# Performance work log

Hardware: AMD Instinct MI355X
Metric: run time of the kernel (lower is better)

The kernel has to match this reference:

```python
import jax, jax.numpy as jnp
import numpy as np
from jax import lax

SHIFT_SIZE = 5
PAD = SHIFT_SIZE // 2


def _shift(xn, axis):
    """xn: (B, C, Hp, Wp, Dp) zero-padded volume. Split channels into
    SHIFT_SIZE chunks and roll each chunk by shift in [-PAD, PAD] along `axis`."""
    chunks = jnp.split(xn, SHIFT_SIZE, axis=1)
    shifted = [jnp.roll(c, s, axis=axis) for c, s in zip(chunks, range(-PAD, PAD + 1))]
    return jnp.concatenate(shifted, axis=1)


def _shift_tokens(x, H, W, D, axis):
    """x: (B, N, C) tokens -> shifted tokens (B, N, C). axis=2 shifts H, axis=3 shifts W."""
    B, N, C = x.shape
    xn = x.transpose(0, 2, 1).reshape(B, C, H, W, D)
    xn = jnp.pad(xn, ((0, 0), (0, 0), (PAD, PAD), (PAD, PAD), (PAD, PAD)))
    xs = _shift(xn, axis)
    xs = xs[:, :, PAD:PAD + H, PAD:PAD + W, PAD:PAD + D]
    return xs.reshape(B, C, N).transpose(0, 2, 1)


def setup_inputs() -> dict:
    key = jax.random.key(0)
    ks = jax.random.split(key, 4)
    B, H, W, D = 2, 32, 32, 32
    N = H * W * D
    Cin, Ch = 160, 640
    return {
        "x": jax.random.normal(ks[0], (B, N, Cin), jnp.float32),
        "fc1_w": jax.random.normal(ks[1], (Ch, Cin), jnp.float32) * 0.02,
        "fc1_b": jnp.zeros((Ch,), jnp.float32),
        "dw_w": jax.random.normal(ks[2], (Ch, 1, 3, 3, 3), jnp.float32) * (2.0 / 27.0) ** 0.5,
        "dw_b": jnp.zeros((Ch,), jnp.float32),
        "fc2_w": jax.random.normal(ks[3], (Cin, Ch), jnp.float32) * 0.02,
        "fc2_b": jnp.zeros((Cin,), jnp.float32),
        "H": H, "W": W, "D": D,
    }


def reference(x, fc1_w, fc1_b, dw_w, dw_b, fc2_w, fc2_b, H, W, D):
    B, N, Cin = x.shape
    Ch = fc1_w.shape[0]
    # shift block 1: roll along H (axis 2)
    xs = _shift_tokens(x, H, W, D, axis=2)
    # fc1
    h = jnp.einsum('bnc,hc->bnh', xs, fc1_w) + fc1_b  # (B, N, Ch)
    # depthwise 3x3x3 conv
    hv = h.transpose(0, 2, 1).reshape(B, Ch, H, W, D)
    hv = lax.conv_general_dilated(
        hv, dw_w, window_strides=(1, 1, 1), padding='SAME',
        feature_group_count=Ch,
        dimension_numbers=('NCDHW', 'OIDHW', 'NCDHW'))
    hv = hv + dw_b[None, :, None, None, None]
    hv = jax.nn.gelu(hv, approximate=False)
    h = hv.reshape(B, Ch, N).transpose(0, 2, 1)
    # shift block 2: roll along W (axis 3)
    hs = _shift_tokens(h, H, W, D, axis=3)
    # fc2
    out = jnp.einsum('bnh,oh->bno', hs, fc2_w) + fc2_b  # (B, N, Cin)
    return out
```

## Files before the change

### kernel.cpp

```cpp
#include <hip/hip_runtime.h>
#include <hip/hip_bf16.h>
#include <math.h>

#define DEVI __device__ __forceinline__

typedef _Float16 f16;
typedef f16 f16x2 __attribute__((ext_vector_type(2)));
typedef f16 f16x4 __attribute__((ext_vector_type(4)));
typedef f16 f16x8 __attribute__((ext_vector_type(8)));
typedef float f32x4 __attribute__((ext_vector_type(4)));

constexpr int Bb = 2, Hh = 32, Ww = 32, Dd = 32;
constexpr int Nn = Hh * Ww * Dd;
constexpr int BN = Bb * Nn;
constexpr int CIN = 160, CHH = 640;
constexpr int PD = 34;
constexpr int PT = PD * PD * PD;

constexpr size_t W1_OFF  = 0;
constexpr size_t W2_OFF  = W1_OFF + (size_t)CHH * CIN * 2;
constexpr size_t WTH_OFF = W2_OFF + (size_t)CIN * CHH * 2;
constexpr size_t ZP_OFF  = WTH_OFF + 34816;
constexpr size_t U_OFF   = 458752;
constexpr size_t H1P_OFF = U_OFF + (size_t)BN * CHH * 2;

DEVI void async16(const void* g, void* l) {
  __builtin_amdgcn_global_load_lds(
      (const __attribute__((address_space(1))) void*)g,
      (__attribute__((address_space(3))) void*)l, 16, 0, 0);
}

__global__ __launch_bounds__(256) void k_prep_w(const float* __restrict__ fc1w,
                                                const float* __restrict__ fc2w,
                                                const float* __restrict__ dww,
                                                f16* __restrict__ w1h,
                                                f16* __restrict__ w2h,
                                                f16* __restrict__ wTh,
                                                unsigned* __restrict__ zp) {
  int i = blockIdx.x * 256 + threadIdx.x;
  const int NW = CHH * CIN;
  if (i < NW) {
    w1h[i] = (f16)fc1w[i];
  } else if (i < 2 * NW) {
    int j = i - NW;
    w2h[j] = (f16)fc2w[j];
  } else if (i < 2 * NW + 27 * CHH) {
    int j = i - 2 * NW;
    int ch = j / 27, tap = j % 27;
    wTh[tap * CHH + ch] = (f16)dww[j];
  } else if (i < 2 * NW + 27 * CHH + 2048) {
    zp[i - (2 * NW + 27 * CHH)] = 0u;
  }
}

__global__ __launch_bounds__(256) void k_zero_pad(f16* __restrict__ h1p) {
  int g = blockIdx.x * 256 + threadIdx.x;
  int p = g / 80;
  int c = g - p * 80;
  if (p >= 2 * PT) return;
  int r = p % PT;
  int hp = r / (PD * PD);
  int r2 = r % (PD * PD);
  int wp = r2 / PD, dp = r2 % PD;
  bool pad = (hp == 0) | (hp == PD - 1) | (wp == 0) | (wp == PD - 1) |
             (dp == 0) | (dp == PD - 1);
  if (!pad) return;
  f16x8 z = {};
  *(f16x8*)&h1p[(size_t)p * CHH + c * 8] = z;
}

__global__ __launch_bounds__(256) void k_gemm1(const float* __restrict__ x,
                                               const f16* __restrict__ w1h,
                                               const float* __restrict__ fc1b,
                                               f16* __restrict__ h1p) {
  constexpr int LDA = 168;
  __shared__ f16 lsA[128 * LDA];
  __shared__ f16 lsB[128 * 32];
  const int tid = threadIdx.x;
  const int lane = tid & 63, wave = tid >> 6;
  const int row0 = blockIdx.x * 128;
  const int wr = wave >> 1, wc = wave & 1;
  const int rl = lane & 15, kb = (lane >> 4) * 8;

#pragma unroll
  for (int i = 0; i < 20; ++i) {
    int c = i * 256 + tid;
    int row = c / 40;
    int q = c - row * 40;
    int ch0 = q * 4;
    int ks = ch0 >> 5;
    int s = ks - 2;
    int t = row0 + row;
    int h = (t >> 10) & 31;
    int hs = h - s;
    float4 v = {0.f, 0.f, 0.f, 0.f};
    if (hs >= 0 && hs < 32)
      v = *(const float4*)&x[(long)(t - s * 1024) * CIN + ch0];
    f16x4 o4;
    o4[0] = (f16)v.x; o4[1] = (f16)v.y; o4[2] = (f16)v.z; o4[3] = (f16)v.w;
    *(f16x4*)&lsA[row * LDA + ch0] = o4;
  }
  __syncthreads();

  for (int nt = 0; nt < 5; ++nt) {
    const int col0 = nt * 128;
    f32x4 acc[4][4] = {};
    for (int ks = 0; ks < 5; ++ks) {
#pragma unroll
      for (int issue = 0; issue < 2; ++issue) {
        int c = issue * 256 + tid;
        int br = c >> 2;
        int kc = (c & 3) * 8;
        const f16* src = w1h + (size_t)(col0 + br) * CIN + ks * 32 + kc;
        async16(src, (char*)lsB + issue * 4096 + wave * 1024);
      }
      __syncthreads();
      f16x8 af[4], bfr[4];
#pragma unroll
      for (int mi = 0; mi < 4; ++mi)
        af[mi] = *(const f16x8*)&lsA[(wr * 64 + mi * 16 + rl) * LDA + ks * 32 + kb];
#pragma unroll
      for (int ni = 0; ni < 4; ++ni)
        bfr[ni] = *(const f16x8*)&lsB[(wc * 64 + ni * 16 + rl) * 32 + kb];
#pragma unroll
      for (int mi = 0; mi < 4; ++mi)
#pragma unroll
        for (int ni = 0; ni < 4; ++ni)
          acc[mi][ni] = __builtin_amdgcn_mfma_f32_16x16x32_f16(af[mi], bfr[ni], acc[mi][ni], 0, 0, 0);
      __syncthreads();
    }
    const int rq = lane >> 4;
#pragma unroll
    for (int mi = 0; mi < 4; ++mi) {
      int rowq = row0 + wr * 64 + mi * 16 + rq * 4;
      int bq = rowq >> 15;
      int nq = rowq & 32767;
      int hq = nq >> 10, wq = (nq >> 5) & 31, dq = nq & 31;
      size_t pos = (size_t)((bq * PD + hq + 1) * PD + (wq + 1)) * PD + (dq + 1);
      f16* dst0 = h1p + pos * CHH;
#pragma unroll
      for (int ni = 0; ni < 4; ++ni) {
        int col = col0 + wc * 64 + ni * 16 + rl;
        float bias = fc1b[col];
#pragma unroll
        for (int r = 0; r < 4; ++r)
          dst0[(size_t)r * CHH + col] = (f16)(acc[mi][ni][r] + bias);
      }
    }
  }
}

__global__ __launch_bounds__(256) void k_conv(const f16* __restrict__ h1p,
                                              const f16* __restrict__ wTh,
                                              const float* __restrict__ dwb,
                                              f16* __restrict__ h2h) {
  __shared__ f16 lw[27 * 64];
  __shared__ f16 lb[64];
  const int tid = threadIdx.x;
  const int cg = blockIdx.y;
#pragma unroll
  for (int i = 0; i < 7; ++i) {
    int idx = i * 256 + tid;
    if (idx < 27 * 64) lw[idx] = wTh[(idx >> 6) * CHH + cg * 64 + (idx & 63)];
  }
  if (tid < 64) lb[tid] = (f16)dwb[cg * 64 + tid];
  __syncthreads();

  const int lane = tid & 63, wave = tid >> 6;
  const int line = blockIdx.x * 4 + wave;
  const int c8 = lane & 7, dq = lane >> 3;
  const int d0 = dq * 4;
  const int ch0 = cg * 64 + c8 * 8;
  const int w = line & 31, h = (line >> 5) & 31, b = line >> 10;

  const size_t cidx = (size_t)((b * PD + h) * PD + w) * PD + d0;
  const f16* base = h1p + cidx * CHH + ch0;

  f16x8 acc[4];
  {
    f16x8 binit = *(const f16x8*)&lb[c8 * 8];
    acc[0] = binit; acc[1] = binit; acc[2] = binit; acc[3] = binit;
  }

#pragma unroll
  for (int kz = 0; kz < 3; ++kz) {
#pragma unroll
    for (int ky = 0; ky < 3; ++ky) {
      const f16* pb = base + (size_t)(kz * PD + ky) * PD * CHH;
      f16x8 wt[3];
#pragma unroll
      for (int kx = 0; kx < 3; ++kx)
        wt[kx] = *(const f16x8*)&lw[((kz * 9 + ky * 3 + kx) << 6) + c8 * 8];
      f16x8 v[6];
#pragma unroll
      for (int j = 0; j < 6; ++j)
        v[j] = *(const f16x8*)(pb + (size_t)j * CHH);
#pragma unroll
      for (int o = 0; o < 4; ++o)
#pragma unroll
        for (int kx = 0; kx < 3; ++kx)
          acc[o] = v[o + kx] * wt[kx] + acc[o];
    }
  }

  const ptrdiff_t obase = (ptrdiff_t)(line * 32 + d0) * CHH + ch0;
#pragma unroll
  for (int o = 0; o < 4; ++o) {
    f16x8 xa = acc[o];
    f16x8 ov;
#pragma unroll
    for (int j = 0; j < 8; j += 2) {
      float g01[2];
#pragma unroll
      for (int u2 = 0; u2 < 2; ++u2) {
        float xv = (float)xa[j + u2];
        float x2 = xv * xv;
        float uu = xv * (2.3022078f + 0.102943324f * x2);
        float e = __builtin_exp2f(uu);
        float r = __builtin_amdgcn_rcpf(1.0f + e);
        g01[u2] = xv - xv * r;
      }
      f16x2 pk = __builtin_bit_cast(f16x2, __builtin_amdgcn_cvt_pkrtz(g01[0], g01[1]));
      ov[j] = pk[0]; ov[j + 1] = pk[1];
    }
    *(f16x8*)&h2h[obase + (ptrdiff_t)o * CHH] = ov;
  }
}

__global__ __launch_bounds__(256) void k_gemm2(const f16* __restrict__ h2h,
                                               const f16* __restrict__ w2h,
                                               const float* __restrict__ fc2b,
                                               const f16* __restrict__ zp,
                                               float* __restrict__ out) {
  __shared__ f16 lsA[128 * 64];
  __shared__ f16 lsB[160 * 64];
  const int tid = threadIdx.x, lane = tid & 63, wave = tid >> 6;
  const int row0 = blockIdx.x * 128;
  const int rl = lane & 15, kb = (lane >> 4) * 8;

  f32x4 acc[2][10] = {};

  for (int kt = 0; kt < 10; ++kt) {
    __syncthreads();
    const int k0 = kt * 64;
    const int s = (k0 >> 7) - 2;
#pragma unroll
    for (int issue = 0; issue < 4; ++issue) {
      int c = issue * 256 + tid;
      int ar = c >> 3;
      int kc = (c & 7) * 8;
      int t = row0 + ar;
      int w = (t >> 5) & 31;
      int wsv = w - s;
      const f16* src;
      if (wsv >= 0 && wsv < 32)
        src = h2h + (size_t)(t - s * 32) * CHH + k0 + kc;
      else
        src = zp + (size_t)(c & 63) * 8;
      async16(src, (char*)lsA + issue * 4096 + wave * 1024);
    }
#pragma unroll
    for (int issue = 0; issue < 5; ++issue) {
      int c = issue * 256 + tid;
      int br = c >> 3;
      int kc = (c & 7) * 8;
      const f16* src = w2h + (size_t)br * CHH + k0 + kc;
      async16(src, (char*)lsB + issue * 4096 + wave * 1024);
    }
    __syncthreads();
#pragma unroll
    for (int kk = 0; kk < 2; ++kk) {
      f16x8 af[2], bfr[10];
#pragma unroll
      for (int mi = 0; mi < 2; ++mi)
        af[mi] = *(const f16x8*)&lsA[(wave * 32 + mi * 16 + rl) * 64 + kk * 32 + kb];
#pragma unroll
      for (int ni = 0; ni < 10; ++ni)
        bfr[ni] = *(const f16x8*)&lsB[(ni * 16 + rl) * 64 + kk * 32 + kb];
#pragma unroll
      for (int mi = 0; mi < 2; ++mi)
#pragma unroll
        for (int ni = 0; ni < 10; ++ni)
          acc[mi][ni] = __builtin_amdgcn_mfma_f32_16x16x32_f16(af[mi], bfr[ni], acc[mi][ni], 0, 0, 0);
    }
  }
  const int rq = lane >> 4;
#pragma unroll
  for (int mi = 0; mi < 2; ++mi) {
#pragma unroll
    for (int ni = 0; ni < 10; ++ni) {
      int col = ni * 16 + rl;
      float bias = fc2b[col];
#pragma unroll
      for (int r = 0; r < 4; ++r) {
        int row = row0 + wave * 32 + mi * 16 + rq * 4 + r;
        out[(size_t)row * CIN + col] = acc[mi][ni][r] + bias;
      }
    }
  }
}

extern "C" void kernel_launch(void* const* d_in, const int* in_sizes, int n_in,
                              void* d_out, int out_size, void* d_ws, size_t ws_size,
                              hipStream_t stream) {
  const float* x    = (const float*)d_in[0];
  const float* fc1w = (const float*)d_in[1];
  const float* fc1b = (const float*)d_in[2];
  const float* dww  = (const float*)d_in[3];
  const float* dwb  = (const float*)d_in[4];
  const float* fc2w = (const float*)d_in[5];
  const float* fc2b = (const float*)d_in[6];

  char* ws = (char*)d_ws;
  f16* w1h  = (f16*)(ws + W1_OFF);
  f16* w2h  = (f16*)(ws + W2_OFF);
  f16* wTh  = (f16*)(ws + WTH_OFF);
  f16* zp   = (f16*)(ws + ZP_OFF);
  f16* h2h  = (f16*)(ws + U_OFF);
  f16* h1p  = (f16*)(ws + H1P_OFF);
  float* out = (float*)d_out;

  k_zero_pad<<<(2 * PT * 80) / 256, 256, 0, stream>>>(h1p);
  k_prep_w<<<876, 256, 0, stream>>>(fc1w, fc2w, dww, w1h, w2h, wTh, (unsigned*)zp);
  k_gemm1<<<512, 256, 0, stream>>>(x, w1h, fc1b, h1p);
  dim3 gc(BN / 32 / 4, 10);
  k_conv<<<gc, 256, 0, stream>>>(h1p, wTh, dwb, h2h);
  k_gemm2<<<512, 256, 0, stream>>>(h2h, w2h, fc2b, zp, out);
}
```

Measured before the change: 141.5 us.

## Load GEMM operands directly from global and merge prep kernels

```diff
diff --git a/kernel.cpp b/kernel.cpp
--- a/kernel.cpp
+++ b/kernel.cpp
@@ -30,31 +30,36 @@
       (__attribute__((address_space(3))) void*)l, 16, 0, 0);
 }
 
-__global__ __launch_bounds__(256) void k_prep_w(const float* __restrict__ fc1w,
-                                                const float* __restrict__ fc2w,
-                                                const float* __restrict__ dww,
-                                                f16* __restrict__ w1h,
-                                                f16* __restrict__ w2h,
-                                                f16* __restrict__ wTh,
-                                                unsigned* __restrict__ zp) {
-  int i = blockIdx.x * 256 + threadIdx.x;
-  const int NW = CHH * CIN;
-  if (i < NW) {
-    w1h[i] = (f16)fc1w[i];
-  } else if (i < 2 * NW) {
-    int j = i - NW;
-    w2h[j] = (f16)fc2w[j];
-  } else if (i < 2 * NW + 27 * CHH) {
-    int j = i - 2 * NW;
-    int ch = j / 27, tap = j % 27;
-    wTh[tap * CHH + ch] = (f16)dww[j];
-  } else if (i < 2 * NW + 27 * CHH + 2048) {
-    zp[i - (2 * NW + 27 * CHH)] = 0u;
-  }
-}
-
-__global__ __launch_bounds__(256) void k_zero_pad(f16* __restrict__ h1p) {
-  int g = blockIdx.x * 256 + threadIdx.x;
+constexpr int PREPW_BLOCKS = 876;
+constexpr int ZPAD_BLOCKS  = (2 * PT * 80 + 255) / 256;
+
+__global__ __launch_bounds__(256) void k_prep(const float* __restrict__ fc1w,
+                                              const float* __restrict__ fc2w,
+                                              const float* __restrict__ dww,
+                                              f16* __restrict__ w1h,
+                                              f16* __restrict__ w2h,
+                                              f16* __restrict__ wTh,
+                                              unsigned* __restrict__ zp,
+                                              f16* __restrict__ h1p) {
+  const int bid = blockIdx.x;
+  const int tid = threadIdx.x;
+  if (bid < PREPW_BLOCKS) {
+    int i = bid * 256 + tid;
+    const int NW = CHH * CIN;
+    if (i < NW) {
+      w1h[i] = (f16)fc1w[i];
+    } else if (i < 2 * NW) {
+      w2h[i - NW] = (f16)fc2w[i - NW];
+    } else if (i < 2 * NW + 27 * CHH) {
+      int j = i - 2 * NW;
+      int ch = j / 27, tap = j % 27;
+      wTh[tap * CHH + ch] = (f16)dww[j];
+    } else if (i < 2 * NW + 27 * CHH + 2048) {
+      zp[i - (2 * NW + 27 * CHH)] = 0u;
+    }
+    return;
+  }
+  int g = (bid - PREPW_BLOCKS) * 256 + tid;
   int p = g / 80;
   int c = g - p * 80;
   if (p >= 2 * PT) return;
@@ -75,7 +80,6 @@
                                                f16* __restrict__ h1p) {
   constexpr int LDA = 168;
   __shared__ f16 lsA[128 * LDA];
-  __shared__ f16 lsB[128 * 32];
   const int tid = threadIdx.x;
   const int lane = tid & 63, wave = tid >> 6;
   const int row0 = blockIdx.x * 128;
@@ -105,29 +109,21 @@
   for (int nt = 0; nt < 5; ++nt) {
     const int col0 = nt * 128;
     f32x4 acc[4][4] = {};
+#pragma unroll
     for (int ks = 0; ks < 5; ++ks) {
-#pragma unroll
-      for (int issue = 0; issue < 2; ++issue) {
-        int c = issue * 256 + tid;
-        int br = c >> 2;
-        int kc = (c & 3) * 8;
-        const f16* src = w1h + (size_t)(col0 + br) * CIN + ks * 32 + kc;
-        async16(src, (char*)lsB + issue * 4096 + wave * 1024);
-      }
-      __syncthreads();
-      f16x8 af[4], bfr[4];
+      f16x8 bfr[4];
+#pragma unroll
+      for (int ni = 0; ni < 4; ++ni)
+        bfr[ni] = *(const f16x8*)&w1h[(size_t)(col0 + wc * 64 + ni * 16 + rl) * CIN + ks * 32 + kb];
+      f16x8 af[4];
 #pragma unroll
       for (int mi = 0; mi < 4; ++mi)
         af[mi] = *(const f16x8*)&lsA[(wr * 64 + mi * 16 + rl) * LDA + ks * 32 + kb];
 #pragma unroll
-      for (int ni = 0; ni < 4; ++ni)
-        bfr[ni] = *(const f16x8*)&lsB[(wc * 64 + ni * 16 + rl) * 32 + kb];
-#pragma unroll
       for (int mi = 0; mi < 4; ++mi)
 #pragma unroll
         for (int ni = 0; ni < 4; ++ni)
           acc[mi][ni] = __builtin_amdgcn_mfma_f32_16x16x32_f16(af[mi], bfr[ni], acc[mi][ni], 0, 0, 0);
-      __syncthreads();
     }
     const int rq = lane >> 4;
 #pragma unroll
@@ -232,51 +228,33 @@
                                                const float* __restrict__ fc2b,
                                                const f16* __restrict__ zp,
                                                float* __restrict__ out) {
-  __shared__ f16 lsA[128 * 64];
-  __shared__ f16 lsB[160 * 64];
   const int tid = threadIdx.x, lane = tid & 63, wave = tid >> 6;
   const int row0 = blockIdx.x * 128;
   const int rl = lane & 15, kb = (lane >> 4) * 8;
 
   f32x4 acc[2][10] = {};
+  const f16* zpl = zp + (size_t)lane * 16;
 
   for (int kt = 0; kt < 10; ++kt) {
-    __syncthreads();
     const int k0 = kt * 64;
-    const int s = (k0 >> 7) - 2;
-#pragma unroll
-    for (int issue = 0; issue < 4; ++issue) {
-      int c = issue * 256 + tid;
-      int ar = c >> 3;
-      int kc = (c & 7) * 8;
-      int t = row0 + ar;
-      int w = (t >> 5) & 31;
-      int wsv = w - s;
-      const f16* src;
-      if (wsv >= 0 && wsv < 32)
-        src = h2h + (size_t)(t - s * 32) * CHH + k0 + kc;
-      else
-        src = zp + (size_t)(c & 63) * 8;
-      async16(src, (char*)lsA + issue * 4096 + wave * 1024);
-    }
-#pragma unroll
-    for (int issue = 0; issue < 5; ++issue) {
-      int c = issue * 256 + tid;
-      int br = c >> 3;
-      int kc = (c & 7) * 8;
-      const f16* src = w2h + (size_t)br * CHH + k0 + kc;
-      async16(src, (char*)lsB + issue * 4096 + wave * 1024);
-    }
-    __syncthreads();
+    const int s = (kt >> 1) - 2;
 #pragma unroll
     for (int kk = 0; kk < 2; ++kk) {
-      f16x8 af[2], bfr[10];
-#pragma unroll
-      for (int mi = 0; mi < 2; ++mi)
-        af[mi] = *(const f16x8*)&lsA[(wave * 32 + mi * 16 + rl) * 64 + kk * 32 + kb];
+      f16x8 af[2];
+#pragma unroll
+      for (int mi = 0; mi < 2; ++mi) {
+        int rowb = row0 + wave * 32 + mi * 16;
+        int w = (rowb >> 5) & 31;
+        int ws = w - s;
+        const f16* pa = ((unsigned)ws < 32u)
+            ? &h2h[(size_t)(rowb - s * 32 + rl) * CHH + k0 + kk * 32 + kb]
+            : zpl;
+        af[mi] = *(const f16x8*)pa;
+      }
+      f16x8 bfr[10];
 #pragma unroll
       for (int ni = 0; ni < 10; ++ni)
-        bfr[ni] = *(const f16x8*)&lsB[(ni * 16 + rl) * 64 + kk * 32 + kb];
+        bfr[ni] = *(const f16x8*)&w2h[(size_t)(ni * 16 + rl) * CHH + k0 + kk * 32 + kb];
 #pragma unroll
       for (int mi = 0; mi < 2; ++mi)
 #pragma unroll
@@ -320,8 +298,8 @@
   f16* h1p  = (f16*)(ws + H1P_OFF);
   float* out = (float*)d_out;
 
-  k_zero_pad<<<(2 * PT * 80) / 256, 256, 0, stream>>>(h1p);
-  k_prep_w<<<876, 256, 0, stream>>>(fc1w, fc2w, dww, w1h, w2h, wTh, (unsigned*)zp);
+  k_prep<<<PREPW_BLOCKS + ZPAD_BLOCKS, 256, 0, stream>>>(
+      fc1w, fc2w, dww, w1h, w2h, wTh, (unsigned*)zp, h1p);
   k_gemm1<<<512, 256, 0, stream>>>(x, w1h, fc1b, h1p);
   dim3 gc(BN / 32 / 4, 10);
   k_conv<<<gc, 256, 0, stream>>>(h1p, wTh, dwb, h2h);
```

After: 189.5 us. +33.9%, slower.
